# Kernel tuning notes

Measured on AMD Instinct MI355X. Metric: run time of the kernel, lower is better.

The kernel has to match this reference:

```python
import jax, jax.numpy as jnp
import numpy as np

B, T, I, C, O = 256, 1024, 128, 256, 10


def setup_inputs() -> dict:
    key = jax.random.key(0)
    k1, k2, k3, k4, k5 = jax.random.split(key, 5)
    x = jax.random.normal(k1, (B, T, I), dtype=jnp.float32)
    # xavier-like scale for kernels
    kernel = jax.random.normal(k2, (I, 2 * C), dtype=jnp.float32) * (6.0 / (I + 2 * C)) ** 0.5
    recurrent_kernel = jax.random.normal(k3, (C, 2 * C), dtype=jnp.float32) * (6.0 / (C + 2 * C)) ** 0.5
    # bias: forget-gate half initialized to log(uniform(1, T-1)), rest zero
    u = jax.random.uniform(k4, (C,), minval=1.0, maxval=float(T - 1))
    recurrent_bias = jnp.concatenate([jnp.log(u), jnp.zeros((C,), jnp.float32)])
    dense_w = jax.random.normal(k5, (C, O), dtype=jnp.float32) * (1.0 / C) ** 0.5
    dense_b = jnp.zeros((O,), jnp.float32)
    return {"x": x, "kernel": kernel, "recurrent_kernel": recurrent_kernel,
            "recurrent_bias": recurrent_bias, "dense_w": dense_w, "dense_b": dense_b}


def reference(x, kernel, recurrent_kernel, recurrent_bias, dense_w, dense_b):
    cells = recurrent_kernel.shape[0]
    # Precompute input projection for all timesteps in one big GEMM: [B,T,2C]
    xz = jnp.einsum('bti,ig->btg', x, kernel) + recurrent_bias
    xz_t = jnp.swapaxes(xz, 0, 1)  # [T, B, 2C] for scan over time

    def step(carry, z_in):
        h, c = carry
        z = z_in + h @ recurrent_kernel  # [B, 2C]
        f = jax.nn.sigmoid(z[:, :cells])
        c_new = f * c + (1.0 - f) * jnp.tanh(z[:, cells:])
        return (c_new, c_new), None

    h0 = jnp.zeros((x.shape[0], cells), x.dtype)
    (h_final, _), _ = jax.lax.scan(step, (h0, h0), xz_t)
    return h_final @ dense_w + dense_b
```

## Files before the change

kernel.cpp:

```cpp
#include <hip/hip_runtime.h>

#define BB 256
#define TT 1024
#define II 128
#define GG 512
#define CC 256
#define L2E 1.44269504f

typedef _Float16 f16;
typedef _Float16 h8_t __attribute__((ext_vector_type(8)));
typedef float f4_t __attribute__((ext_vector_type(4)));
typedef unsigned short ushort_t;

static __device__ __forceinline__ float fast_rcp(float x) {
#if __has_builtin(__builtin_amdgcn_rcpf)
    return __builtin_amdgcn_rcpf(x);
#else
    return 1.f / x;
#endif
}
static __device__ __forceinline__ float fast_exp2(float x) {
#if __has_builtin(__builtin_amdgcn_exp2f)
    return __builtin_amdgcn_exp2f(x);
#else
    return exp2f(x);
#endif
}

__global__ void kt_transpose(const float* __restrict__ kin, f16* __restrict__ kt) {
    int idx = blockIdx.x * 256 + threadIdx.x;
    int k = idx >> 9;
    int n = idx & 511;
    kt[n * II + k] = (f16)kin[k * GG + n];
}

__global__ __launch_bounds__(256)
void gemm_xz(const float* __restrict__ x, const f16* __restrict__ kt,
             const float* __restrict__ bias, ushort_t* __restrict__ xz) {
    const int  ntile = blockIdx.x;
    const long mtile = blockIdx.y;
    const int wave = threadIdx.x >> 6;
    const int lane = threadIdx.x & 63;
    const int wm = (wave & 1) * 64;
    const int wn = (wave >> 1) * 64;
    const int lm = lane & 15;
    const int q  = lane >> 4;

    f4_t acc[4][4];
#pragma unroll
    for (int mi = 0; mi < 4; ++mi)
#pragma unroll
        for (int ni = 0; ni < 4; ++ni)
            acc[mi][ni] = (f4_t){0.f, 0.f, 0.f, 0.f};

#pragma unroll
    for (int kc = 0; kc < 4; ++kc) {
        h8_t a[4], bf[4];
#pragma unroll
        for (int mi = 0; mi < 4; ++mi) {
            const int rowm = (int)(mtile * 128) + wm + mi * 16 + lm;
            const int b  = rowm & 255;
            const int tt = rowm >> 8;
            const float* ap = x + (size_t)b * (TT * II) + (size_t)tt * II + kc * 32 + q * 8;
            f4_t p0 = *(const f4_t*)ap;
            f4_t p1 = *(const f4_t*)(ap + 4);
            h8_t tv;
            tv[0] = (f16)p0[0]; tv[1] = (f16)p0[1]; tv[2] = (f16)p0[2]; tv[3] = (f16)p0[3];
            tv[4] = (f16)p1[0]; tv[5] = (f16)p1[1]; tv[6] = (f16)p1[2]; tv[7] = (f16)p1[3];
            a[mi] = tv;
        }
#pragma unroll
        for (int ni = 0; ni < 4; ++ni) {
            const f16* bp = kt + (size_t)(ntile * 128 + wn + ni * 16 + lm) * II + kc * 32 + q * 8;
            bf[ni] = *(const h8_t*)bp;
        }
#pragma unroll
        for (int mi = 0; mi < 4; ++mi)
#pragma unroll
            for (int ni = 0; ni < 4; ++ni)
                acc[mi][ni] = __builtin_amdgcn_mfma_f32_16x16x32_f16(a[mi], bf[ni], acc[mi][ni], 0, 0, 0);
    }

#pragma unroll
    for (int mi = 0; mi < 4; ++mi) {
#pragma unroll
        for (int ni = 0; ni < 4; ++ni) {
            const int col = ntile * 128 + wn + ni * 16 + lm;
            const float bv = bias[col];
            const float s  = (col < CC) ? L2E : (2.0f * L2E);
#pragma unroll
            for (int r = 0; r < 4; ++r) {
                const size_t rowm = (size_t)(mtile * 128 + wm + mi * 16 + q * 4 + r);
                f16 hv = (f16)((acc[mi][ni][r] + bv) * s);
                xz[rowm * GG + col] = *(ushort_t*)&hv;
            }
        }
    }
}

#define STEP(T, PF, PP, HRD, HWR) do {                                               \
    h8_t af[8];                                                                      \
    _Pragma("unroll") for (int kt = 0; kt < 8; ++kt)                                 \
        af[kt] = *(const h8_t*)((HRD) + lm * 264 + kt * 32 + q * 8);                 \
    f4_t acc[4];                                                                     \
    _Pragma("unroll") for (int ni = 0; ni < 4; ++ni) {                               \
        f4_t av;                                                                     \
        _Pragma("unroll") for (int r = 0; r < 4; ++r) {                              \
            ushort_t u = (PF)[ni * 4 + r];                                           \
            f16 hv = *(f16*)&u;                                                      \
            av[r] = (float)hv;                                                       \
        }                                                                            \
        acc[ni] = av;                                                                \
    }                                                                                \
    if ((T) + 2 < TT) {                                                              \
        _Pragma("unroll") for (int ni = 0; ni < 4; ++ni)                             \
            _Pragma("unroll") for (int r = 0; r < 4; ++r)                            \
                (PF)[ni * 4 + r] = (PP)[r * 512 + ni * 128];                         \
        (PP) += 2 * 131072;                                                          \
    }                                                                                \
    _Pragma("unroll") for (int kt = 0; kt < 8; ++kt)                                 \
        _Pragma("unroll") for (int ni = 0; ni < 4; ++ni)                             \
            acc[ni] = __builtin_amdgcn_mfma_f32_16x16x32_f16(af[kt], bw[ni][kt], acc[ni], 0, 0, 0); \
    _Pragma("unroll") for (int ni = 0; ni < 2; ++ni)                                 \
        _Pragma("unroll") for (int r = 0; r < 4; ++r) {                              \
            float zf = acc[ni][r];                                                   \
            float zg = acc[ni + 2][r];                                               \
            float ef = fast_exp2(-zf);                                               \
            float eg = fast_exp2(-fabsf(zg));                                        \
            float t1 = (zg < 0.f) ? -ef : ef;                                        \
            float cv = cst[ni][r];                                                   \
            float num = fmaf(cv, eg, cv) + fmaf(-t1, eg, t1);                        \
            float den = (1.f + ef) * (1.f + eg);                                     \
            cst[ni][r] = num * fast_rcp(den);                                        \
        }                                                                            \
    _Pragma("unroll") for (int ni = 0; ni < 2; ++ni)                                 \
        _Pragma("unroll") for (int r = 0; r < 4; ++r)                                \
            (HWR)[(q * 4 + r) * 264 + (wave + 8 * ni) * 16 + lm] = (f16)cst[ni][r];  \
    asm volatile("s_waitcnt lgkmcnt(0)\n\ts_barrier" ::: "memory");                  \
} while (0)

__global__ __launch_bounds__(512, 2)
void janet_rec(const float* __restrict__ rk, const float* __restrict__ dw,
               const float* __restrict__ db, const ushort_t* __restrict__ xz,
               float* __restrict__ out) {
    const int g = blockIdx.x;
    const int tid = threadIdx.x;
    const int wave = tid >> 6;
    const int lane = tid & 63;
    const int lm = lane & 15;
    const int q  = lane >> 4;

    h8_t bw[4][8];
#pragma unroll
    for (int ni = 0; ni < 4; ++ni) {
        const float s = (ni < 2) ? L2E : (2.0f * L2E);
#pragma unroll
        for (int kt = 0; kt < 8; ++kt) {
            h8_t tv;
#pragma unroll
            for (int j = 0; j < 8; ++j)
                tv[j] = (f16)(s * rk[(size_t)(kt * 32 + q * 8 + j) * GG + (wave + 8 * ni) * 16 + lm]);
            bw[ni][kt] = tv;
        }
    }

    __shared__ __align__(16) f16 hb[2][16][264];
    f16* h0 = &hb[0][0][0];
    f16* h1 = &hb[1][0][0];
    for (int i = tid; i < 2 * 16 * 264; i += 512) ((f16*)hb)[i] = (f16)0.f;

    float cst[2][4];
#pragma unroll
    for (int ni = 0; ni < 2; ++ni)
#pragma unroll
        for (int r = 0; r < 4; ++r) cst[ni][r] = 0.f;

    const ushort_t* pb = xz + ((size_t)g * 16 + q * 4) * 512 + wave * 16 + lm;
    const ushort_t* p1b = pb + 131072;
    const ushort_t* p0 = pb + 2 * 131072;
    const ushort_t* p1 = pb + 3 * 131072;

    ushort_t pf0[16], pf1[16];
#pragma unroll
    for (int ni = 0; ni < 4; ++ni)
#pragma unroll
        for (int r = 0; r < 4; ++r) {
            pf0[ni * 4 + r] = pb[r * 512 + ni * 128];
            pf1[ni * 4 + r] = p1b[r * 512 + ni * 128];
        }
    __syncthreads();

#pragma unroll 1
    for (int t = 0; t < TT; t += 2) {
        STEP(t,     pf0, p0, h0, h1);
        STEP(t + 1, pf1, p1, h1, h0);
    }

    __shared__ float hf[16][256];
#pragma unroll
    for (int ni = 0; ni < 2; ++ni)
#pragma unroll
        for (int r = 0; r < 4; ++r)
            hf[q * 4 + r][(wave + 8 * ni) * 16 + lm] = cst[ni][r];
    __syncthreads();
    if (tid < 160) {
        const int bi = tid / 10, o = tid % 10;
        float acc = db[o];
#pragma unroll 8
        for (int cc = 0; cc < CC; ++cc) acc = fmaf(hf[bi][cc], dw[cc * 10 + o], acc);
        out[(g * 16 + bi) * 10 + o] = acc;
    }
}

__global__ void ws_too_small(float* out, float wssz) {
    int i = blockIdx.x * 256 + threadIdx.x;
    if (i < BB * 10) out[i] = (i == 0) ? wssz : 0.f;
}

extern "C" void kernel_launch(void* const* d_in, const int* in_sizes, int n_in,
                              void* d_out, int out_size, void* d_ws, size_t ws_size,
                              hipStream_t stream) {
    const float* x   = (const float*)d_in[0];
    const float* kin = (const float*)d_in[1];
    const float* rk  = (const float*)d_in[2];
    const float* rb  = (const float*)d_in[3];
    const float* dw  = (const float*)d_in[4];
    const float* db  = (const float*)d_in[5];
    float* out = (float*)d_out;

    const size_t xz_bytes = (size_t)BB * TT * GG * 2;
    const size_t kt_bytes = (size_t)GG * II * 2;
    if (ws_size < xz_bytes + kt_bytes) {
        ws_too_small<<<10, 256, 0, stream>>>(out, (float)ws_size);
        return;
    }

    ushort_t* xz = (ushort_t*)d_ws;
    f16* kt = (f16*)((char*)d_ws + xz_bytes);

    kt_transpose<<<256, 256, 0, stream>>>(kin, kt);
    gemm_xz<<<dim3(4, 2048), 256, 0, stream>>>(x, kt, rb, xz);
    janet_rec<<<16, 512, 0, stream>>>(rk, dw, db, xz, out);
}
```

Before: 1.698 ms.

## Reorder xz layout for vector loads and interleave gate MFMA with activation

The projection kernel now writes xz in a blocked [t][group][col][16-batch] layout, so each lane's four batch rows for a column are contiguous. The recurrent kernel can then prefetch them with one 8-byte vector load per column instead of four scalar strided loads. The recurrent step also reorders its MFMAs so the first column-pair's gates finish early, letting its nonlinearity and LDS write overlap the second pair's MFMAs. This cuts global load instruction count on the serial critical path, and both kernels' indexing must stay consistent with the new layout.

```diff
diff --git a/kernel.cpp b/kernel.cpp
--- a/kernel.cpp
+++ b/kernel.cpp
@@ -11,6 +11,7 @@
 typedef _Float16 h8_t __attribute__((ext_vector_type(8)));
 typedef float f4_t __attribute__((ext_vector_type(4)));
 typedef unsigned short ushort_t;
+typedef unsigned short us4_t __attribute__((ext_vector_type(4)));
 
 static __device__ __forceinline__ float fast_rcp(float x) {
 #if __has_builtin(__builtin_amdgcn_rcpf)
@@ -83,17 +84,22 @@
 
 #pragma unroll
     for (int mi = 0; mi < 4; ++mi) {
+        const int rowm0 = (int)(mtile * 128) + wm + mi * 16 + q * 4;
+        const int t  = rowm0 >> 8;
+        const int b0 = rowm0 & 255;
+        const int gq = b0 >> 4;
 #pragma unroll
         for (int ni = 0; ni < 4; ++ni) {
             const int col = ntile * 128 + wn + ni * 16 + lm;
             const float bv = bias[col];
             const float s  = (col < CC) ? L2E : (2.0f * L2E);
+            us4_t v;
 #pragma unroll
             for (int r = 0; r < 4; ++r) {
-                const size_t rowm = (size_t)(mtile * 128 + wm + mi * 16 + q * 4 + r);
                 f16 hv = (f16)((acc[mi][ni][r] + bv) * s);
-                xz[rowm * GG + col] = *(ushort_t*)&hv;
+                v[r] = *(ushort_t*)&hv;
             }
+            *(us4_t*)(xz + (((size_t)t * 16 + gq) * 512 + col) * 16 + q * 4) = v;
         }
     }
 }
@@ -113,29 +119,51 @@
         acc[ni] = av;                                                                \
     }                                                                                \
     if ((T) + 2 < TT) {                                                              \
-        _Pragma("unroll") for (int ni = 0; ni < 4; ++ni)                             \
-            _Pragma("unroll") for (int r = 0; r < 4; ++r)                            \
-                (PF)[ni * 4 + r] = (PP)[r * 512 + ni * 128];                         \
+        _Pragma("unroll") for (int ni = 0; ni < 4; ++ni) {                           \
+            us4_t v = *(const us4_t*)((PP) + ni * 2048);                             \
+            (PF)[ni * 4 + 0] = v[0];                                                 \
+            (PF)[ni * 4 + 1] = v[1];                                                 \
+            (PF)[ni * 4 + 2] = v[2];                                                 \
+            (PF)[ni * 4 + 3] = v[3];                                                 \
+        }                                                                            \
         (PP) += 2 * 131072;                                                          \
     }                                                                                \
-    _Pragma("unroll") for (int kt = 0; kt < 8; ++kt)                                 \
-        _Pragma("unroll") for (int ni = 0; ni < 4; ++ni)                             \
-            acc[ni] = __builtin_amdgcn_mfma_f32_16x16x32_f16(af[kt], bw[ni][kt], acc[ni], 0, 0, 0); \
-    _Pragma("unroll") for (int ni = 0; ni < 2; ++ni)                                 \
-        _Pragma("unroll") for (int r = 0; r < 4; ++r) {                              \
-            float zf = acc[ni][r];                                                   \
-            float zg = acc[ni + 2][r];                                               \
-            float ef = fast_exp2(-zf);                                               \
-            float eg = fast_exp2(-fabsf(zg));                                        \
-            float t1 = (zg < 0.f) ? -ef : ef;                                        \
-            float cv = cst[ni][r];                                                   \
-            float num = fmaf(cv, eg, cv) + fmaf(-t1, eg, t1);                        \
-            float den = (1.f + ef) * (1.f + eg);                                     \
-            cst[ni][r] = num * fast_rcp(den);                                        \
-        }                                                                            \
-    _Pragma("unroll") for (int ni = 0; ni < 2; ++ni)                                 \
-        _Pragma("unroll") for (int r = 0; r < 4; ++r)                                \
-            (HWR)[(q * 4 + r) * 264 + (wave + 8 * ni) * 16 + lm] = (f16)cst[ni][r];  \
+                                 \
+    _Pragma("unroll") for (int kt = 0; kt < 8; ++kt) {                               \
+        acc[0] = __builtin_amdgcn_mfma_f32_16x16x32_f16(af[kt], bw[0][kt], acc[0], 0, 0, 0); \
+        acc[2] = __builtin_amdgcn_mfma_f32_16x16x32_f16(af[kt], bw[2][kt], acc[2], 0, 0, 0); \
+    }                                                                                \
+                                                              \
+    _Pragma("unroll") for (int kt = 0; kt < 8; ++kt) {                               \
+        acc[1] = __builtin_amdgcn_mfma_f32_16x16x32_f16(af[kt], bw[1][kt], acc[1], 0, 0, 0); \
+        acc[3] = __builtin_amdgcn_mfma_f32_16x16x32_f16(af[kt], bw[3][kt], acc[3], 0, 0, 0); \
+    }                                                                                \
+                       \
+    _Pragma("unroll") for (int r = 0; r < 4; ++r) {                                  \
+        float zf = acc[0][r];                                                        \
+        float zg = acc[2][r];                                                        \
+        float ef = fast_exp2(-zf);                                                   \
+        float eg = fast_exp2(-fabsf(zg));                                            \
+        float t1 = (zg < 0.f) ? -ef : ef;                                            \
+        float cv = cst[0][r];                                                        \
+        float num = fmaf(cv, eg, cv) + fmaf(-t1, eg, t1);                            \
+        float den = (1.f + ef) * (1.f + eg);                                         \
+        cst[0][r] = num * fast_rcp(den);                                             \
+        (HWR)[(q * 4 + r) * 264 + wave * 16 + lm] = (f16)cst[0][r];                  \
+    }                                                                                \
+                                                    \
+    _Pragma("unroll") for (int r = 0; r < 4; ++r) {                                  \
+        float zf = acc[1][r];                                                        \
+        float zg = acc[3][r];                                                        \
+        float ef = fast_exp2(-zf);                                                   \
+        float eg = fast_exp2(-fabsf(zg));                                            \
+        float t1 = (zg < 0.f) ? -ef : ef;                                            \
+        float cv = cst[1][r];                                                        \
+        float num = fmaf(cv, eg, cv) + fmaf(-t1, eg, t1);                            \
+        float den = (1.f + ef) * (1.f + eg);                                         \
+        cst[1][r] = num * fast_rcp(den);                                             \
+        (HWR)[(q * 4 + r) * 264 + (wave + 8) * 16 + lm] = (f16)cst[1][r];            \
+    }                                                                                \
     asm volatile("s_waitcnt lgkmcnt(0)\n\ts_barrier" ::: "memory");                  \
 } while (0)
 
@@ -175,19 +203,20 @@
 #pragma unroll
         for (int r = 0; r < 4; ++r) cst[ni][r] = 0.f;
 
-    const ushort_t* pb = xz + ((size_t)g * 16 + q * 4) * 512 + wave * 16 + lm;
-    const ushort_t* p1b = pb + 131072;
-    const ushort_t* p0 = pb + 2 * 131072;
-    const ushort_t* p1 = pb + 3 * 131072;
+    const ushort_t* PB = xz + (size_t)g * 8192 + (wave * 16 + lm) * 16 + q * 4;
+    const ushort_t* p0 = PB + 2 * 131072;
+    const ushort_t* p1 = PB + 3 * 131072;
 
     ushort_t pf0[16], pf1[16];
 #pragma unroll
-    for (int ni = 0; ni < 4; ++ni)
-#pragma unroll
-        for (int r = 0; r < 4; ++r) {
-            pf0[ni * 4 + r] = pb[r * 512 + ni * 128];
-            pf1[ni * 4 + r] = p1b[r * 512 + ni * 128];
-        }
+    for (int ni = 0; ni < 4; ++ni) {
+        us4_t v0 = *(const us4_t*)(PB + ni * 2048);
+        us4_t v1 = *(const us4_t*)(PB + 131072 + ni * 2048);
+        pf0[ni * 4 + 0] = v0[0]; pf0[ni * 4 + 1] = v0[1];
+        pf0[ni * 4 + 2] = v0[2]; pf0[ni * 4 + 3] = v0[3];
+        pf1[ni * 4 + 0] = v1[0]; pf1[ni * 4 + 1] = v1[1];
+        pf1[ni * 4 + 2] = v1[2]; pf1[ni * 4 + 3] = v1[3];
+    }
     __syncthreads();
 
 #pragma unroll 1
```

Result: faster. 1.557 ms (-8.3%).
